# Kernel tuning notes

Hardware: AMD Instinct MI355X
Metric: run time of the kernel (lower is better)

Reference implementation:

```python
import jax, jax.numpy as jnp
import numpy as np

# The torch module draws rot/shifts/flips from a seeded torch RNG. Torch RNG
# streams cannot be reproduced in JAX, so the sampled augmentation parameters
# are frozen to fixed, in-range constants (rot in {0,40,...,320}, shifts in
# [-20,20], flips subset of dims (2,3)). The math of the transform is faithful.
ROT_DEG = 80.0          # rotations[2]
SHIFTS = (7, -13)       # torch.randint(-20, 21, (2,)) -> roll dims (1, 2)
FLIP_AXES = (2, 3)      # subset of torch.arange(2, 4) selected by coin flips


def setup_inputs() -> dict:
    key = jax.random.key(0)
    x = jax.random.normal(key, (2, 128, 128, 128, 8), dtype=jnp.float32)
    return {"x": x}


def _rotate_hw(x, angle_deg):
    """Rotate x=[B,H,W,D,F] in the (H,W) plane by angle_deg (CCW positive),
    nearest-neighbor sampling about the image center, zero fill outside.
    This matches torchvision.transforms.functional.rotate defaults applied
    per [D,H,W] slice in the original, fully vectorized over B, D, F."""
    B, H, W, D, F = x.shape
    theta = jnp.deg2rad(jnp.float32(angle_deg))
    cy, cx = (H - 1) * 0.5, (W - 1) * 0.5
    yy, xx = jnp.meshgrid(
        jnp.arange(H, dtype=jnp.float32),
        jnp.arange(W, dtype=jnp.float32),
        indexing="ij",
    )
    dy, dx = yy - cy, xx - cx
    c, s = jnp.cos(theta), jnp.sin(theta)
    # inverse mapping: output pixel (y, x) pulls from source (sy, sx)
    sx = c * dx - s * dy + cx
    sy = s * dx + c * dy + cy
    iy = jnp.round(sy).astype(jnp.int32)
    ix = jnp.round(sx).astype(jnp.int32)
    valid = (iy >= 0) & (iy < H) & (ix >= 0) & (ix < W)  # [H, W]
    iyc = jnp.clip(iy, 0, H - 1)
    ixc = jnp.clip(ix, 0, W - 1)
    out = x[:, iyc, ixc]  # gather -> [B, H, W, D, F]
    return jnp.where(valid[None, :, :, None, None], out, jnp.float32(0.0))


def reference(x):
    # fused batched rotate + roll + flip (augment_features path, x.dim()==5)
    y = _rotate_hw(x, ROT_DEG)
    y = jnp.roll(y, SHIFTS, axis=(1, 2))
    y = jnp.flip(y, axis=FLIP_AXES)
    return y
```

## Files before the change

kernel.cpp:

```cpp
#include <hip/hip_runtime.h>
#include <math.h>


__global__ __launch_bounds__(256) void Augment_77532749627421_kernel(
    const float* __restrict__ x, float* __restrict__ out,
    const float c, const float s, const long total4)
{
    const float cc = 63.5f;
    long idx    = (long)blockIdx.x * blockDim.x + threadIdx.x;
    long stride = (long)gridDim.x * blockDim.x;
    for (long o4 = idx; o4 < total4; o4 += stride) {
        int f4 = (int)(o4 & 1);
        int d  = (int)((o4 >> 1) & 127);
        int j  = (int)((o4 >> 8) & 127);
        int i  = (int)((o4 >> 15) & 127);
        int b  = (int)(o4 >> 22);

        int i1 = (i - 7) & 127;
        int j1 = (140 - j) & 127;

        float dx = (float)j1 - cc;
        float dy = (float)i1 - cc;
        float sx = __fadd_rn(__fsub_rn(__fmul_rn(c, dx), __fmul_rn(s, dy)), cc);
        float sy = __fadd_rn(__fadd_rn(__fmul_rn(s, dx), __fmul_rn(c, dy)), cc);
        int ix = (int)rintf(sx);
        int iy = (int)rintf(sy);

        float4 v = make_float4(0.f, 0.f, 0.f, 0.f);
        if (((unsigned)ix < 128u) && ((unsigned)iy < 128u)) {
            int dsrc = 127 - d;
            long src4 = ((((long)b * 128 + iy) * 128 + ix) * 128 + dsrc) * 2 + f4;
            v = ((const float4*)x)[src4];
        }
        ((float4*)out)[o4] = v;
    }
}

extern "C" void kernel_launch(void* const* d_in, const int* in_sizes, int n_in,
                              void* d_out, int out_size, void* d_ws, size_t ws_size,
                              hipStream_t stream) {
    const float* x = (const float*)d_in[0];
    float* out = (float*)d_out;

    float deg2rad_c = (float)(M_PI / 180.0);
    float theta = 80.0f * deg2rad_c;
    float c = (float)cos((double)theta);
    float s = (float)sin((double)theta);

    long total4 = (long)out_size / 4;
    int block = 256;
    int grid = 2048;
    hipLaunchKernelGGL(Augment_77532749627421_kernel, dim3(grid), dim3(block), 0, stream,
                       x, out, c, s, total4);
}
```

Measured before the change: 44.66 us.

## Assign one wavefront per output pixel slab with hoisted rotation math and nontemporal stores

Adds a specialized kernel where each wavefront copies two full 4KB pixel slabs (D×F). The rotation and roll index math is done once per pixel instead of once per float4, and each lane issues several independent loads before storing. Stores are nontemporal to avoid polluting the cache, and the grid is sized exactly instead of grid-stride looping. The original grid-stride kernel is kept as a fallback for shapes that don't divide evenly.

Measured after the change: 41.86 us (median of 2 runs). 1.07x faster.

```diff
diff --git a/kernel.cpp b/kernel.cpp
--- a/kernel.cpp
+++ b/kernel.cpp
@@ -2,7 +2,57 @@
 #include <math.h>
 
 
-__global__ __launch_bounds__(256) void Augment_77532749627421_kernel(
+typedef float f32x4 __attribute__((ext_vector_type(4)));
+
+__global__ __launch_bounds__(256) void Augment_slab(
+    const f32x4* __restrict__ x4, f32x4* __restrict__ out4,
+    const float c, const float s)
+{
+    const float cc = 63.5f;
+    const int lane = threadIdx.x & 63;
+    const int wid  = threadIdx.x >> 6;
+    const int p0 = (blockIdx.x * 4 + wid) * 2;
+
+    f32x4 v[2][4];
+#pragma unroll
+    for (int t = 0; t < 2; ++t) {
+        const int p = p0 + t;
+        const int j = p & 127;
+        const int i = (p >> 7) & 127;
+        const int b = p >> 14;
+
+        const int i1 = (i - 7) & 127;
+        const int j1 = (140 - j) & 127;
+        const float dx = (float)j1 - cc;
+        const float dy = (float)i1 - cc;
+        const float sx = __fadd_rn(__fsub_rn(__fmul_rn(c, dx), __fmul_rn(s, dy)), cc);
+        const float sy = __fadd_rn(__fadd_rn(__fmul_rn(s, dx), __fmul_rn(c, dy)), cc);
+        const int ixs = (int)rintf(sx);
+        const int iys = (int)rintf(sy);
+        const bool ok = ((unsigned)ixs < 128u) && ((unsigned)iys < 128u);
+
+#pragma unroll
+        for (int k = 0; k < 4; ++k) v[t][k] = (f32x4)(0.f);
+        if (ok) {
+            const long srcbase = (((long)b * 16384) + (long)iys * 128 + ixs) * 256;
+#pragma unroll
+            for (int k = 0; k < 4; ++k) {
+                const int q = k * 64 + lane;
+                const int srcq = 254 - q + 2 * (q & 1);
+                v[t][k] = x4[srcbase + srcq];
+            }
+        }
+    }
+#pragma unroll
+    for (int t = 0; t < 2; ++t) {
+        const long dstbase = (long)(p0 + t) * 256;
+#pragma unroll
+        for (int k = 0; k < 4; ++k)
+            __builtin_nontemporal_store(v[t][k], &out4[dstbase + k * 64 + lane]);
+    }
+}
+
+__global__ __launch_bounds__(256) void Augment_generic(
     const float* __restrict__ x, float* __restrict__ out,
     const float c, const float s, const long total4)
 {
@@ -15,21 +65,17 @@
         int j  = (int)((o4 >> 8) & 127);
         int i  = (int)((o4 >> 15) & 127);
         int b  = (int)(o4 >> 22);
-
         int i1 = (i - 7) & 127;
         int j1 = (140 - j) & 127;
-
         float dx = (float)j1 - cc;
         float dy = (float)i1 - cc;
         float sx = __fadd_rn(__fsub_rn(__fmul_rn(c, dx), __fmul_rn(s, dy)), cc);
         float sy = __fadd_rn(__fadd_rn(__fmul_rn(s, dx), __fmul_rn(c, dy)), cc);
-        int ix = (int)rintf(sx);
-        int iy = (int)rintf(sy);
-
+        int ixs = (int)rintf(sx);
+        int iys = (int)rintf(sy);
         float4 v = make_float4(0.f, 0.f, 0.f, 0.f);
-        if (((unsigned)ix < 128u) && ((unsigned)iy < 128u)) {
-            int dsrc = 127 - d;
-            long src4 = ((((long)b * 128 + iy) * 128 + ix) * 128 + dsrc) * 2 + f4;
+        if (((unsigned)ixs < 128u) && ((unsigned)iys < 128u)) {
+            long src4 = ((((long)b * 128 + iys) * 128 + ixs) * 128 + (127 - d)) * 2 + f4;
             v = ((const float4*)x)[src4];
         }
         ((float4*)out)[o4] = v;
@@ -48,8 +94,13 @@
     float s = (float)sin((double)theta);
 
     long total4 = (long)out_size / 4;
-    int block = 256;
-    int grid = 2048;
-    hipLaunchKernelGGL(Augment_77532749627421_kernel, dim3(grid), dim3(block), 0, stream,
-                       x, out, c, s, total4);
+    long pixels = total4 / 256;
+    if ((long)out_size % 1024 == 0 && pixels % 8 == 0) {
+        int grid = (int)(pixels / 8);
+        hipLaunchKernelGGL(Augment_slab, dim3(grid), dim3(256), 0, stream,
+                           (const f32x4*)x, (f32x4*)out, c, s);
+    } else {
+        hipLaunchKernelGGL(Augment_generic, dim3(2048), dim3(256), 0, stream,
+                           x, out, c, s, total4);
+    }
 }
```
